# Optimization experiments

Hardware: AMD Instinct MI355X
Metric: run time of the kernel (lower is better)

Reference implementation:

```python
import jax, jax.numpy as jnp
import numpy as np

H = 96  # hidden size


def setup_inputs() -> dict:
    key = jax.random.key(0)
    ks = jax.random.split(key, 7)
    T, B = 16384, 32
    s = 1.0 / np.sqrt(H)
    return {
        "x": jax.random.normal(ks[0], (T, B, 1), dtype=jnp.float32),
        "w_ih": jax.random.normal(ks[1], (4 * H, 1), dtype=jnp.float32) * s,
        "w_hh": jax.random.normal(ks[2], (4 * H, H), dtype=jnp.float32) * s,
        "b_ih": jax.random.normal(ks[3], (4 * H,), dtype=jnp.float32) * s,
        "b_hh": jax.random.normal(ks[4], (4 * H,), dtype=jnp.float32) * s,
        "fc_w": jax.random.normal(ks[5], (1, H), dtype=jnp.float32) * s,
        "fc_b": jax.random.normal(ks[6], (1,), dtype=jnp.float32) * s,
    }


def reference(x, w_ih, w_hh, b_ih, b_hh, fc_w, fc_b):
    # x: [T, B, 1] (time-major, like nn.LSTM with batch_first=False)
    T, B, _ = x.shape
    res = x[:, :, 0:1]
    # Precompute the input contribution to the gates for all timesteps: [T, B, 4H]
    gates_x = jnp.einsum('tbi,gi->tbg', x, w_ih) + b_ih + b_hh

    def step(carry, gx):
        h, c = carry  # [B, H] each
        g = gx + h @ w_hh.T  # [B, 4H]
        i, f, gg, o = jnp.split(g, 4, axis=-1)  # PyTorch gate order i|f|g|o
        i = jax.nn.sigmoid(i)
        f = jax.nn.sigmoid(f)
        gg = jnp.tanh(gg)
        o = jax.nn.sigmoid(o)
        c = f * c + i * gg
        h = o * jnp.tanh(c)
        return (h, c), h

    h0 = jnp.zeros((B, H), dtype=x.dtype)  # hidden=None -> zero init
    c0 = jnp.zeros((B, H), dtype=x.dtype)
    _, hs = jax.lax.scan(step, (h0, c0), gates_x)  # hs: [T, B, H]
    # FullyConnected(x) + residual
    return jnp.einsum('tbh,oh->tbo', hs, fc_w) + fc_b + res
```

## Files before the change

### kernel.cpp

```cpp
#include <hip/hip_runtime.h>


constexpr int HH   = 96;
constexpr int BB   = 32;
constexpr int TT   = 16384;
constexpr int TH   = 384;
constexpr int NS   = 512;
constexpr int ROWP = 104;

typedef _Float16 f16x8 __attribute__((ext_vector_type(8)));
typedef _Float16 f16x2 __attribute__((ext_vector_type(2)));
typedef float    f32x4 __attribute__((ext_vector_type(4)));

template <int CTRL>
__device__ __forceinline__ float dpp_bcast(float v) {
    int r = __builtin_amdgcn_mov_dpp(__builtin_bit_cast(int, v), CTRL, 0xF, 0xF, true);
    return __builtin_bit_cast(float, r);
}
constexpr int DPP_B1 = 0x55;
constexpr int DPP_B2 = 0xAA;
constexpr int DPP_B3 = 0xFF;

#define LOG2E 1.44269504f

__attribute__((amdgpu_flat_work_group_size(TH, TH)))
__global__ void lstm_kernel(const float* __restrict__ x,
                            const float* __restrict__ w_ih,
                            const float* __restrict__ w_hh,
                            const float* __restrict__ b_ih,
                            const float* __restrict__ b_hh,
                            const float* __restrict__ fc_w,
                            const float* __restrict__ fc_b,
                            float* __restrict__ out) {
    __shared__ __align__(16) _Float16 hist[(NS + 1) * ROWP];
    __shared__ __align__(16) float xs[NS];
    __shared__ float fcw_s[HH];

    const int tid = threadIdx.x;
    const int b   = blockIdx.x;
    const int wv  = tid >> 6;
    const int l   = tid & 63;
    const int h16 = l >> 4;
    const int rIn = l & 15;
    const int s   = rIn & 3;
    const int q   = rIn >> 2;
    const int j   = 16 * wv + 4 * h16 + q;

    const float ek_s = (s == 2) ? (-2.0f * LOG2E) : (-LOG2E);
    f16x8 Bw[4][3];
#pragma unroll
    for (int t = 0; t < 4; ++t) {
        const float* wrow = w_hh + (s * HH + 16 * wv + 4 * t + q) * HH;
#pragma unroll
        for (int kt = 0; kt < 3; ++kt) {
            const float* wr = wrow + kt * 32 + 8 * h16;
            f16x8 v;
#pragma unroll
            for (int e = 0; e < 8; ++e) v[e] = (_Float16)(wr[e] * ek_s);
            Bw[t][kt] = v;
        }
    }
#pragma unroll
    for (int t = 0; t < 4; ++t)
#pragma unroll
        for (int kt = 0; kt < 3; ++kt) asm volatile("" : "+v"(Bw[t][kt]));

    const float wih2  = w_ih[s * HH + j] * ek_s;
    const float bias2 = (b_ih[s * HH + j] + b_hh[s * HH + j]) * ek_s;
    const float a_mul = (s == 2) ? (-4.0f * LOG2E) : 1.0f;
    const float a_add = (s == 2) ? (2.0f * LOG2E) : 0.0f;
    const bool  t1 = (h16 == 1), t2 = (h16 == 2), t3 = (h16 == 3);

    const float fcb = fc_b[0];
    float c = 0.0f;

    for (int i = tid; i < HH; i += TH) fcw_s[i] = fc_w[i];

    auto flush = [&](int t0) {
        for (int i = tid; i < NS; i += TH) {
            const uint2* hr = (const uint2*)(hist + (i + 1) * ROWP);
            float a = 0.0f;
#pragma unroll
            for (int m = 0; m < 24; ++m) {
                uint2 u = hr[m];
                f16x2 p0 = __builtin_bit_cast(f16x2, u.x);
                f16x2 p1 = __builtin_bit_cast(f16x2, u.y);
                a = fmaf((float)p0.x, fcw_s[4 * m + 0], a);
                a = fmaf((float)p0.y, fcw_s[4 * m + 1], a);
                a = fmaf((float)p1.x, fcw_s[4 * m + 2], a);
                a = fmaf((float)p1.y, fcw_s[4 * m + 3], a);
            }
            out[(t0 + i) * BB + b] = a + fcb + xs[i];
        }
    };

    const _Float16* rd_p;
    _Float16*       wr_p;

    auto step = [&](float gx, const int ofs) {
        const uint4* p = (const uint4*)(rd_p + ofs);
        uint4 u0 = p[0], u1 = p[4], u2 = p[8];
        const f16x8 a0 = __builtin_bit_cast(f16x8, u0);
        const f16x8 a1 = __builtin_bit_cast(f16x8, u1);
        const f16x8 a2 = __builtin_bit_cast(f16x8, u2);

        f32x4 acc[4] = {{0.f, 0.f, 0.f, 0.f}, {0.f, 0.f, 0.f, 0.f},
                        {0.f, 0.f, 0.f, 0.f}, {0.f, 0.f, 0.f, 0.f}};
#pragma unroll
        for (int t = 0; t < 4; ++t)
            acc[t] = __builtin_amdgcn_mfma_f32_16x16x32_f16(a0, Bw[t][0], acc[t], 0, 0, 0);
#pragma unroll
        for (int t = 0; t < 4; ++t)
            acc[t] = __builtin_amdgcn_mfma_f32_16x16x32_f16(a1, Bw[t][1], acc[t], 0, 0, 0);
#pragma unroll
        for (int t = 0; t < 4; ++t)
            acc[t] = __builtin_amdgcn_mfma_f32_16x16x32_f16(a2, Bw[t][2], acc[t], 0, 0, 0);

        float v = t1 ? acc[1][0] : acc[0][0];
        v       = t2 ? acc[2][0] : v;
        v       = t3 ? acc[3][0] : v;

        const float pre = v + gx;
        const float act =
            fmaf(__builtin_amdgcn_rcpf(1.0f + __builtin_amdgcn_exp2f(pre)),
                 a_mul, a_add);
        const float fv = dpp_bcast<DPP_B1>(act);
        const float gv = dpp_bcast<DPP_B2>(act);
        const float ov = dpp_bcast<DPP_B3>(act);
        c = fmaf(fv, c, act * gv);
        const float rt = __builtin_amdgcn_rcpf(1.0f + __builtin_amdgcn_exp2f(c));
        const float h  = fmaf(ov + ov, rt, -ov);
        if (s == 0) *(wr_p + ofs) = (_Float16)h;
        __syncthreads();
    };

    for (int w = 0; w < TT / NS; ++w) {
        const int t0 = w * NS;
        if (w == 0) {
            if (tid < 48) ((uint32_t*)hist)[tid] = 0u;
        } else {
            flush(t0 - NS);
            if (tid < 48)
                ((uint32_t*)hist)[tid] = ((const uint32_t*)(hist + NS * ROWP))[tid];
        }
        __syncthreads();
        for (int i = tid; i < NS; i += TH) xs[i] = x[(t0 + i) * BB + b];
        __syncthreads();

        rd_p = hist + 8 * h16;
        wr_p = hist + ROWP + j;
        for (int tt = 0; tt < NS; tt += 4) {
            const float4 xq = *(const float4*)(xs + tt);
            const float gx0 = fmaf(xq.x, wih2, bias2);
            const float gx1 = fmaf(xq.y, wih2, bias2);
            const float gx2 = fmaf(xq.z, wih2, bias2);
            const float gx3 = fmaf(xq.w, wih2, bias2);
            step(gx0, 0 * ROWP);
            step(gx1, 1 * ROWP);
            step(gx2, 2 * ROWP);
            step(gx3, 3 * ROWP);
            rd_p += 4 * ROWP;
            wr_p += 4 * ROWP;
        }
    }
    flush(TT - NS);
}

extern "C" void kernel_launch(void* const* d_in, const int* in_sizes, int n_in,
                              void* d_out, int out_size, void* d_ws, size_t ws_size,
                              hipStream_t stream) {
    const float* x    = (const float*)d_in[0];
    const float* w_ih = (const float*)d_in[1];
    const float* w_hh = (const float*)d_in[2];
    const float* b_ih = (const float*)d_in[3];
    const float* b_hh = (const float*)d_in[4];
    const float* fc_w = (const float*)d_in[5];
    const float* fc_b = (const float*)d_in[6];
    float* out = (float*)d_out;

    lstm_kernel<<<dim3(BB), dim3(TH), 0, stream>>>(x, w_ih, w_hh, b_ih, b_hh,
                                                   fc_w, fc_b, out);
}
```

Before: 5.142 ms.

## Pack two batch recurrences per workgroup with per-half LDS atomic barriers

Each workgroup now runs two batch elements, one per 384-thread half, for 768 threads over 16 blocks. The block-wide __syncthreads is replaced by a per-half spin barrier built on LDS atomic counters, so the two independent recurrences can interleave on one CU and hide each other's latency. The history window drops from 512 to 256 steps so both buffers fit in LDS, which doubles the number of flushes. Spin-waiting waves use issue slots and LDS bandwidth, and the number of active CUs is halved.

```diff
diff --git a/kernel.cpp b/kernel.cpp
--- a/kernel.cpp
+++ b/kernel.cpp
@@ -4,8 +4,10 @@
 constexpr int HH   = 96;
 constexpr int BB   = 32;
 constexpr int TT   = 16384;
-constexpr int TH   = 384;
-constexpr int NS   = 512;
+constexpr int THH  = 384;
+constexpr int TH   = 768;
+constexpr int NB   = 16;
+constexpr int NS   = 256;
 constexpr int ROWP = 104;
 
 typedef _Float16 f16x8 __attribute__((ext_vector_type(8)));
@@ -32,19 +34,40 @@
                             const float* __restrict__ fc_w,
                             const float* __restrict__ fc_b,
                             float* __restrict__ out) {
-    __shared__ __align__(16) _Float16 hist[(NS + 1) * ROWP];
-    __shared__ __align__(16) float xs[NS];
-    __shared__ float fcw_s[HH];
-
-    const int tid = threadIdx.x;
-    const int b   = blockIdx.x;
-    const int wv  = tid >> 6;
-    const int l   = tid & 63;
-    const int h16 = l >> 4;
-    const int rIn = l & 15;
-    const int s   = rIn & 3;
-    const int q   = rIn >> 2;
-    const int j   = 16 * wv + 4 * h16 + q;
+    __shared__ __align__(16) _Float16 hist[2][(NS + 1) * ROWP];
+    __shared__ __align__(16) float xs[2][NS];
+    __shared__ float fcw_s[2][HH];
+    __shared__ int ctr[2][32];
+
+    const int tid  = threadIdx.x;
+    const int dom  = (tid >= THH) ? 1 : 0;
+    const int stid = tid - dom * THH;
+    const int b    = blockIdx.x * 2 + dom;
+    const int wv   = stid >> 6;
+    const int l    = stid & 63;
+    const int h16  = l >> 4;
+    const int rIn  = l & 15;
+    const int s    = rIn & 3;
+    const int q    = rIn >> 2;
+    const int j    = 16 * wv + 4 * h16 + q;
+
+    if (tid < 2) ctr[tid][0] = 0;
+    __syncthreads();
+
+    _Float16* __restrict__ histh = hist[dom];
+    float*    __restrict__ xsh   = xs[dom];
+    float*    __restrict__ fcwd  = fcw_s[dom];
+    int* myctr = &ctr[dom][0];
+
+    int epoch = 0;
+    auto dsync = [&]() {
+        ++epoch;
+        if ((stid & 63) == 0)
+            __hip_atomic_fetch_add(myctr, 1, __ATOMIC_RELEASE,
+                                   __HIP_MEMORY_SCOPE_WORKGROUP);
+        while (__hip_atomic_load(myctr, __ATOMIC_ACQUIRE,
+                                 __HIP_MEMORY_SCOPE_WORKGROUP) < 6 * epoch) {}
+    };
 
     const float ek_s = (s == 2) ? (-2.0f * LOG2E) : (-LOG2E);
     f16x8 Bw[4][3];
@@ -74,23 +97,23 @@
     const float fcb = fc_b[0];
     float c = 0.0f;
 
-    for (int i = tid; i < HH; i += TH) fcw_s[i] = fc_w[i];
+    for (int i = stid; i < HH; i += THH) fcwd[i] = fc_w[i];
 
     auto flush = [&](int t0) {
-        for (int i = tid; i < NS; i += TH) {
-            const uint2* hr = (const uint2*)(hist + (i + 1) * ROWP);
+        for (int i = stid; i < NS; i += THH) {
+            const uint2* hr = (const uint2*)(histh + (i + 1) * ROWP);
             float a = 0.0f;
 #pragma unroll
             for (int m = 0; m < 24; ++m) {
                 uint2 u = hr[m];
                 f16x2 p0 = __builtin_bit_cast(f16x2, u.x);
                 f16x2 p1 = __builtin_bit_cast(f16x2, u.y);
-                a = fmaf((float)p0.x, fcw_s[4 * m + 0], a);
-                a = fmaf((float)p0.y, fcw_s[4 * m + 1], a);
-                a = fmaf((float)p1.x, fcw_s[4 * m + 2], a);
-                a = fmaf((float)p1.y, fcw_s[4 * m + 3], a);
+                a = fmaf((float)p0.x, fcwd[4 * m + 0], a);
+                a = fmaf((float)p0.y, fcwd[4 * m + 1], a);
+                a = fmaf((float)p1.x, fcwd[4 * m + 2], a);
+                a = fmaf((float)p1.y, fcwd[4 * m + 3], a);
             }
-            out[(t0 + i) * BB + b] = a + fcb + xs[i];
+            out[(t0 + i) * BB + b] = a + fcb + xsh[i];
         }
     };
 
@@ -131,26 +154,27 @@
         const float rt = __builtin_amdgcn_rcpf(1.0f + __builtin_amdgcn_exp2f(c));
         const float h  = fmaf(ov + ov, rt, -ov);
         if (s == 0) *(wr_p + ofs) = (_Float16)h;
-        __syncthreads();
+        dsync();
     };
 
     for (int w = 0; w < TT / NS; ++w) {
         const int t0 = w * NS;
         if (w == 0) {
-            if (tid < 48) ((uint32_t*)hist)[tid] = 0u;
+            if (stid < 48) ((uint32_t*)histh)[stid] = 0u;
         } else {
             flush(t0 - NS);
-            if (tid < 48)
-                ((uint32_t*)hist)[tid] = ((const uint32_t*)(hist + NS * ROWP))[tid];
-        }
-        __syncthreads();
-        for (int i = tid; i < NS; i += TH) xs[i] = x[(t0 + i) * BB + b];
-        __syncthreads();
-
-        rd_p = hist + 8 * h16;
-        wr_p = hist + ROWP + j;
+            if (stid < 48)
+                ((uint32_t*)histh)[stid] =
+                    ((const uint32_t*)(histh + NS * ROWP))[stid];
+        }
+        dsync();
+        for (int i = stid; i < NS; i += THH) xsh[i] = x[(t0 + i) * BB + b];
+        dsync();
+
+        rd_p = histh + 8 * h16;
+        wr_p = histh + ROWP + j;
         for (int tt = 0; tt < NS; tt += 4) {
-            const float4 xq = *(const float4*)(xs + tt);
+            const float4 xq = *(const float4*)(xsh + tt);
             const float gx0 = fmaf(xq.x, wih2, bias2);
             const float gx1 = fmaf(xq.y, wih2, bias2);
             const float gx2 = fmaf(xq.z, wih2, bias2);
@@ -178,6 +202,6 @@
     const float* fc_b = (const float*)d_in[6];
     float* out = (float*)d_out;
 
-    lstm_kernel<<<dim3(BB), dim3(TH), 0, stream>>>(x, w_ih, w_hh, b_ih, b_hh,
+    lstm_kernel<<<dim3(NB), dim3(TH), 0, stream>>>(x, w_ih, w_hh, b_ih, b_hh,
                                                    fc_w, fc_b, out);
 }
```

Measured after the change: 6.623 ms. 28.8% more time.
